# Kernel optimization log

Measured on AMD Instinct MI355X. Metric: run time of the kernel, lower is better.

## Reference

```python
import jax, jax.numpy as jnp
import numpy as np

N, H, L, S, E, D = 2, 8, 2048, 2048, 64, 64
C, K, BITS, ITERS = 128, 32, 32, 10
TEMP = 1.0 / np.sqrt(E)  # softmax_temp default 1/sqrt(E)


def setup_inputs() -> dict:
    key = jax.random.key(0)
    k1, k2, k3, k4 = jax.random.split(key, 4)
    return {
        "queries": jax.random.normal(k1, (N, L, H, E), jnp.float32),
        "keys": jax.random.normal(k2, (N, S, H, E), jnp.float32),
        "values": jax.random.normal(k3, (N, S, H, D), jnp.float32),
        "planes": jax.random.normal(k4, (BITS, E + 1), jnp.float32),
    }


def _cluster(bits):
    """K-means (Lloyd) on hamming distance over hash bits. bits: [N,H,L,B] in {0,1}."""
    qsum = bits.sum(-1)  # [N,H,L]
    idx0 = jnp.linspace(0, L - 1, C).astype(jnp.int32)  # deterministic centroid init
    cbits0 = bits[:, :, idx0, :]  # [N,H,C,B]

    def assign(cbits):
        # hamming(x,c) = sum(x) + sum(c) - 2*x.c  for 0/1 bits
        d = qsum[..., None] + cbits.sum(-1)[:, :, None, :] \
            - 2.0 * jnp.einsum('nhlb,nhcb->nhlc', bits, cbits)
        return jnp.argmin(d, -1)  # [N,H,L]

    def body(cbits, _):
        cl = assign(cbits)
        oh = jax.nn.one_hot(cl, C, dtype=bits.dtype)       # [N,H,L,C]
        counts = oh.sum(2)                                  # [N,H,C]
        bs = jnp.einsum('nhlc,nhlb->nhcb', oh, bits)        # per-cluster bit sums
        newc = (2.0 * bs > counts[..., None]).astype(bits.dtype)  # majority vote
        newc = jnp.where(counts[..., None] > 0, newc, cbits)      # keep empty clusters
        return newc, None

    cbits, _ = jax.lax.scan(body, cbits0, None, length=ITERS)
    cl = assign(cbits)
    counts = jax.nn.one_hot(cl, C, dtype=jnp.float32).sum(2)
    return cl, counts


def reference(queries, keys, values, planes):
    q = queries.transpose(0, 2, 1, 3)  # [N,H,L,E]
    k = keys.transpose(0, 2, 1, 3)     # [N,H,S,E]
    v = values.transpose(0, 2, 1, 3)   # [N,H,S,D]

    # LSH hashing of queries
    proj = jnp.einsum('nhle,be->nhlb', q, planes[:, :E]) + planes[:, E]
    bits = (proj > 0).astype(jnp.float32)
    cl, counts = _cluster(bits)  # [N,H,L], [N,H,C]

    sorted_indx = jnp.argsort(cl, axis=-1)
    sorted_cl = jnp.take_along_axis(cl, sorted_indx, -1)
    sq = jnp.take_along_axis(q, sorted_indx[..., None], 2)  # queries sorted by cluster

    # grouped queries = per-cluster mean
    counts_safe = jnp.maximum(counts, 1.0)
    oh = jax.nn.one_hot(cl, C, dtype=q.dtype)
    Qg = jnp.einsum('nhlc,nhle->nhce', oh, q) / counts_safe[..., None]

    # centroid-key dot products and top-k key selection per cluster
    QK = jnp.einsum('nhce,nhse->nhcs', Qg, k)  # [N,H,C,S]
    topk_values, topk = jax.lax.top_k(QK, K)   # [N,H,C,K]

    # bottom-k attention (dense per-cluster, top-k positions zeroed)
    A_full = jax.nn.softmax(TEMP * QK, -1)
    iN = jnp.arange(N)[:, None, None, None]
    iH = jnp.arange(H)[None, :, None, None]
    iC = jnp.arange(C)[None, None, :, None]
    mask = jnp.zeros_like(QK).at[iN, iH, iC, topk].set(1.0)
    A_b = A_full * (1.0 - mask)
    A_bottomk = A_b.sum(-1)                              # [N,H,C]
    Vb_g = jnp.einsum('nhcs,nhsd->nhcd', A_b, v)         # [N,H,C,D]
    Vb = jnp.take_along_axis(Vb_g, sorted_cl[..., None], 2)   # broadcast to queries
    A_bk_q = jnp.take_along_axis(A_bottomk, sorted_cl, 2)     # [N,H,L]

    # exact top-k attention per query
    topk_q = jnp.take_along_axis(topk, sorted_cl[..., None], 2)  # [N,H,L,K]
    gather = jax.vmap(jax.vmap(lambda t, i: t[i]))  # over N,H
    K_sel = gather(k, topk_q)  # [N,H,L,K,E]
    V_sel = gather(v, topk_q)  # [N,H,L,K,D]
    QKs = jnp.einsum('nhle,nhlke->nhlk', sq, K_sel)
    inf_mask = jnp.isinf(topk_values[:, 0, 0, :])  # [N,K] (padding sentinel; all False here)
    QKs = jnp.where(inf_mask[:, None, None, :], -jnp.inf, QKs)
    A_s = jax.nn.softmax(TEMP * QKs, -1) * (1.0 - A_bk_q[..., None])
    Vt = jnp.einsum('nhlk,nhlkd->nhld', A_s, V_sel)

    # combine and undo the cluster sort
    Vs = Vt + Vb
    rev = jnp.argsort(sorted_indx, -1)
    V_new = jnp.take_along_axis(Vs, rev[..., None], 2)
    sparse_index = jnp.take_along_axis(topk_q, rev[..., None], 2)
    A_topk = jnp.take_along_axis(A_s, rev[..., None], 2)
    return V_new.transpose(0, 2, 1, 3), sparse_index, A_topk
```

## Files before the change

### kernel.cpp

```cpp
#include <hip/hip_runtime.h>
#include <math.h>

constexpr int cN = 2, cH = 8, cL = 2048, cS = 2048, cE = 64, cD = 64;
constexpr int cC = 128, cK = 32, cB = 32, cIT = 10;
constexpr int cNH = cN * cH;
constexpr int SK = 8;
constexpr int CHUNK = cS / SK;
constexpr int NT = 16;
constexpr int HW = cC * 33;
constexpr int PARTSZ = 16;
constexpr int SLOTS = 256;
constexpr int NBUF = cIT + 1;

__global__ __launch_bounds__(256)
void k_bits(const float* __restrict__ q, const float* __restrict__ planes,
            unsigned int* __restrict__ bits, int* __restrict__ ghist)
{
    __shared__ float pl[cB * 68];
    int tid = threadIdx.x;
    for (int i = tid; i < cB * (cE + 1); i += 256) {
        int b = i / 65, e = i % 65;
        pl[b * 68 + e] = planes[i];
    }
    {
        const int ZS = NBUF * cNH * HW / 128;
        for (int i = tid; i < ZS; i += 256) ghist[(size_t)blockIdx.x * ZS + i] = 0;
    }
    __syncthreads();
    int idx = blockIdx.x * 256 + tid;
    int l = idx % cL, h = (idx / cL) % cH, n = idx / (cL * cH);
    const float* qr = q + (((size_t)n * cL + l) * cH + h) * cE;
    float qv[cE];
#pragma unroll
    for (int e4 = 0; e4 < cE / 4; ++e4) {
        float4 f = ((const float4*)qr)[e4];
        qv[4*e4+0] = f.x; qv[4*e4+1] = f.y; qv[4*e4+2] = f.z; qv[4*e4+3] = f.w;
    }
    unsigned int w = 0;
    for (int b = 0; b < cB; ++b) {
        const float4* pr = (const float4*)(pl + b * 68);
        float acc = 0.f;
#pragma unroll
        for (int e4 = 0; e4 < cE / 4; ++e4) {
            float4 f = pr[e4];
            acc = fmaf(qv[4*e4+0], f.x, acc);
            acc = fmaf(qv[4*e4+1], f.y, acc);
            acc = fmaf(qv[4*e4+2], f.z, acc);
            acc = fmaf(qv[4*e4+3], f.w, acc);
        }
        acc += pl[b * 68 + 64];
        if (acc > 0.f) w |= (1u << b);
    }
    bits[idx] = w;
}

__global__ __launch_bounds__(128)
void k_lloyd(const unsigned int* __restrict__ bits, int* __restrict__ ghist,
             unsigned int* __restrict__ cents, int* __restrict__ cl,
             int* __restrict__ pcounts, int it)
{
    __shared__ unsigned int scb[cC] __attribute__((aligned(16)));
    __shared__ int hist[HW];
    int tid = threadIdx.x, lane = tid & 63;
    int tile = blockIdx.x & (NT - 1), nh = blockIdx.x / NT;
    if (it == 0) {
        if (tid < cC) {
            int i0 = (int)(((double)tid * 2047.0) / 127.0);
            scb[tid] = bits[(size_t)nh * cL + i0];
        }
    } else {
        const unsigned int* cp = cents + (size_t)(it - 1) * cNH * cC + nh * cC;
        const int* gb = ghist + (size_t)((it - 1) * cNH + nh) * HW;
        if (tid < cC) {
            unsigned int oldc = cp[tid];
            int cnt = gb[4096 + tid];
            if (cnt > 0) {
                unsigned int nw = 0;
#pragma unroll
                for (int b = 0; b < cB; ++b)
                    if (2 * gb[tid * 32 + b] > cnt) nw |= (1u << b);
                oldc = nw;
            }
            scb[tid] = oldc;
        }
    }
    if (it < cIT) {
        for (int i = tid; i < HW; i += 128) hist[i] = 0;
    } else {
        hist[4096 + tid] = 0;
    }
    int l = tile * 128 + tid;
    unsigned int w = bits[(size_t)nh * cL + l];
    unsigned long long mymb = 0ull;
    if (it < cIT) {
#pragma unroll
        for (int b = 0; b < cB; ++b) {
            unsigned long long m = __ballot((w >> b) & 1u);
            if ((lane & 31) == b) mymb = m;
        }
    }
    __syncthreads();
    if (tile == 0 && it < cIT && tid < cC)
        cents[(size_t)it * cNH * cC + nh * cC + tid] = scb[tid];
    const uint4* scb4 = (const uint4*)scb;
    int b0 = 0x7fffffff, b1 = 0x7fffffff, b2 = 0x7fffffff, b3 = 0x7fffffff;
    for (int c4 = 0; c4 < cC / 4; ++c4) {
        uint4 cb = scb4[c4];
        int c = c4 * 4;
        b0 = min(b0, (__popc(w ^ cb.x) << 8) | c);
        b1 = min(b1, (__popc(w ^ cb.y) << 8) | (c + 1));
        b2 = min(b2, (__popc(w ^ cb.z) << 8) | (c + 2));
        b3 = min(b3, (__popc(w ^ cb.w) << 8) | (c + 3));
    }
    int best = min(min(b0, b1), min(b2, b3));
    int bc = best & 255;
    if (it == cIT) cl[(size_t)nh * cL + l] = bc;
    if (it < cIT) {
        unsigned long long rem = ~0ull;
        while (rem) {
            int src = __ffsll((long long)rem) - 1;
            int c = __shfl(bc, src);
            unsigned long long m = __ballot(bc == c);
            if (lane < cB) {
                int contrib = __popcll(m & mymb);
                if (contrib) atomicAdd(&hist[c * 32 + lane], contrib);
            }
            if (lane == 63) atomicAdd(&hist[4096 + c], __popcll(m));
            rem &= ~m;
        }
        __syncthreads();
        int* gb = ghist + (size_t)(it * cNH + nh) * HW;
        for (int i = tid; i < HW; i += 128) {
            int v = hist[i];
            if (v) atomicAdd(&gb[i], v);
        }
    } else {
        unsigned long long rem = ~0ull;
        while (rem) {
            int src = __ffsll((long long)rem) - 1;
            int c = __shfl(bc, src);
            unsigned long long m = __ballot(bc == c);
            if (lane == 63) atomicAdd(&hist[4096 + c], __popcll(m));
            rem &= ~m;
        }
        __syncthreads();
        pcounts[(nh * NT + tile) * cC + tid] = hist[4096 + tid];
    }
}

__global__ __launch_bounds__(128)
void k_rank(const int* __restrict__ cl, const int* __restrict__ pcounts,
            int* __restrict__ counts, int* __restrict__ moff,
            int* __restrict__ sched, int* __restrict__ mlist)
{
    __shared__ int pre[cC];
    __shared__ int scn[cC];
    __shared__ int sbefore[cC];
    __shared__ int wcnt0[cC];
    int tid = threadIdx.x, lane = tid & 63, wid = tid >> 6;
    int tile = blockIdx.x & (NT - 1), nh = blockIdx.x / NT;
    if (tid < cC) {
        int tot = 0, bef = 0;
        for (int t = 0; t < NT; ++t) {
            int v = pcounts[(nh * NT + t) * cC + tid];
            if (t < tile) bef += v;
            tot += v;
        }
        scn[tid] = tot;
        sbefore[tid] = bef;
    }
    __syncthreads();
    if (tid == 0) {
        int run = 0;
        for (int i = 0; i < cC; ++i) { pre[i] = run; run += scn[i]; }
    }
    __syncthreads();
    if (tile == 0) {
        if (tid < cC) {
            counts[nh * cC + tid] = scn[tid];
            moff[nh * cC + tid] = pre[tid];
        }
        sched[nh * SLOTS + tid] = -1;
        sched[nh * SLOTS + 128 + tid] = -1;
        __syncthreads();
        if (tid == 0) {
            int slot = 0;
            for (int i = 0; i < cC; ++i) {
                int np = (scn[i] + PARTSZ - 1) / PARTSZ;
                for (int p = 0; p < np; ++p)
                    sched[nh * SLOTS + slot++] = i | (p << 8);
            }
        }
    }
    int l = tile * 128 + tid;
    int bc = cl[(size_t)nh * cL + l];
    unsigned long long ltmask = (1ull << lane) - 1ull;
    int myrank = 0;
    for (int c = 0; c < cC; ++c) {
        unsigned long long m = __ballot(bc == c);
        if (wid == 0 && lane == 0) wcnt0[c] = __popcll(m);
        if (bc == c) myrank = __popcll(m & ltmask);
    }
    __syncthreads();
    int off = pre[bc] + sbefore[bc] + myrank + (wid == 1 ? wcnt0[bc] : 0);
    mlist[(size_t)nh * cL + off] = l;
}

__global__ __launch_bounds__(64)
void k_qg(const float* __restrict__ q, const int* __restrict__ mlist,
          const int* __restrict__ moff, const int* __restrict__ counts,
          float* __restrict__ Qg)
{
    int b = blockIdx.x;
    int nh = b >> 7;
    int h = nh % cH, n = nh / cH;
    int lane = threadIdx.x;
    int off = moff[b];
    int cnt = counts[b];
    const int* ml = mlist + (size_t)nh * cL + off;
    const float* qb = q + ((size_t)n * cL * cH + h) * cE + lane;
    float acc = 0.f;
    int j = 0;
    for (; j + 4 <= cnt; j += 4) {
        int i0 = ml[j], i1 = ml[j + 1], i2 = ml[j + 2], i3 = ml[j + 3];
        float v0 = qb[(size_t)i0 * cH * cE];
        float v1 = qb[(size_t)i1 * cH * cE];
        float v2 = qb[(size_t)i2 * cH * cE];
        float v3 = qb[(size_t)i3 * cH * cE];
        acc += v0; acc += v1; acc += v2; acc += v3;
    }
    for (; j < cnt; ++j) acc += qb[(size_t)ml[j] * cH * cE];
    float cs = (float)(cnt > 0 ? cnt : 1);
    Qg[(size_t)b * cE + lane] = acc / cs;
}

__global__ __launch_bounds__(256)
void k_qk_gemm(const float* __restrict__ key, const float* __restrict__ Qg,
               float* __restrict__ QK)
{
    __shared__ float qgT[cE][cC + 2];
    __shared__ float kT[cE][128 + 2];
    int tid = threadIdx.x;
    int bs = blockIdx.x & 15;
    int nh = blockIdx.x >> 4;
    int h = nh % cH, n = nh / cH;
    const float4* qsrc = (const float4*)(Qg + (size_t)nh * cC * cE);
#pragma unroll
    for (int i = 0; i < 8; ++i) {
        int f = tid + 256 * i;
        int c = f >> 4, e4 = (f & 15) << 2;
        float4 v = qsrc[f];
        qgT[e4+0][c] = v.x; qgT[e4+1][c] = v.y; qgT[e4+2][c] = v.z; qgT[e4+3][c] = v.w;
    }
    const float* kb = key + (size_t)n * cS * cH * cE + (size_t)h * cE;
    int s0 = bs * 128;
#pragma unroll
    for (int i = 0; i < 8; ++i) {
        int f = tid + 256 * i;
        int s = f >> 4, e4 = (f & 15) << 2;
        float4 v = *(const float4*)(kb + (size_t)(s0 + s) * (cH * cE) + e4);
        kT[e4+0][s] = v.x; kT[e4+1][s] = v.y; kT[e4+2][s] = v.z; kT[e4+3][s] = v.w;
    }
    __syncthreads();
    int tx = tid & 15, ty = tid >> 4;
    float acc[8][8];
#pragma unroll
    for (int i = 0; i < 8; ++i)
#pragma unroll
        for (int j = 0; j < 8; ++j) acc[i][j] = 0.f;
    for (int e = 0; e < cE; ++e) {
        float qv[8], kv[8];
#pragma unroll
        for (int i = 0; i < 8; ++i) qv[i] = qgT[e][ty + 16 * i];
#pragma unroll
        for (int j = 0; j < 8; ++j) kv[j] = kT[e][tx + 16 * j];
#pragma unroll
        for (int i = 0; i < 8; ++i)
#pragma unroll
            for (int j = 0; j < 8; ++j)
                acc[i][j] = fmaf(qv[i], kv[j], acc[i][j]);
    }
    float* dst = QK + (size_t)nh * cC * cS + s0;
#pragma unroll
    for (int i = 0; i < 8; ++i)
#pragma unroll
        for (int j = 0; j < 8; ++j)
            dst[(size_t)(ty + 16 * i) * cS + tx + 16 * j] = acc[i][j];
}

__global__ __launch_bounds__(256)
void k_sel(float* __restrict__ QK, int* __restrict__ topk,
           float* __restrict__ abk)
{
    __shared__ int sbins[4 * 257];
    __shared__ int ired[4];
    __shared__ float fred[4];
    __shared__ unsigned skey[cK];
    __shared__ float sval[cK];
    __shared__ int sidx[cK];
    __shared__ int stopk[cK];
    __shared__ int sDig, sRem, scnt;
    __shared__ float sM;
    int tid = threadIdx.x, lane = tid & 63, wid = tid >> 6;
    int b = blockIdx.x;
    float* qrow = QK + (size_t)b * cS;
    float v[8]; unsigned key[8];
#pragma unroll
    for (int j = 0; j < 8; ++j) {
        float f = qrow[tid + j * 256];
        v[j] = f;
        unsigned u = __float_as_uint(f);
        key[j] = (u & 0x80000000u) ? ~u : (u | 0x80000000u);
    }
    if (tid == 0) { sRem = cK; scnt = 0; }
    unsigned pfx = 0;
    for (int pass = 0; pass < 4; ++pass) {
        int sh = 24 - 8 * pass;
        for (int i = tid; i < 4 * 257; i += 256) sbins[i] = 0;
        __syncthreads();
        int rem = sRem;
#pragma unroll
        for (int j = 0; j < 8; ++j) {
            bool cand = (pass == 0) || ((key[j] >> (sh + 8)) == pfx);
            if (cand) atomicAdd(&sbins[wid * 257 + ((key[j] >> sh) & 255)], 1);
        }
        __syncthreads();
        if (wid == 0) {
            int d0 = lane * 4;
            int c0 = sbins[d0] + sbins[257 + d0] + sbins[514 + d0] + sbins[771 + d0];
            int c1 = sbins[d0+1] + sbins[257+d0+1] + sbins[514+d0+1] + sbins[771+d0+1];
            int c2 = sbins[d0+2] + sbins[257+d0+2] + sbins[514+d0+2] + sbins[771+d0+2];
            int c3 = sbins[d0+3] + sbins[257+d0+3] + sbins[514+d0+3] + sbins[771+d0+3];
            int tot = c0 + c1 + c2 + c3;
            int incl = tot;
#pragma unroll
            for (int off = 1; off < 64; off <<= 1) {
                int o = __shfl_down(incl, off);
                if (lane + off < 64) incl += o;
            }
            int sufHi = incl - tot;
            int G3 = sufHi, G2 = sufHi + c3, G1 = G2 + c2, G0 = G1 + c1;
            int hit = -1, hG = 0;
            if (G0 < rem && rem <= G0 + c0) { hit = d0 + 0; hG = G0; }
            if (G1 < rem && rem <= G1 + c1) { hit = d0 + 1; hG = G1; }
            if (G2 < rem && rem <= G2 + c2) { hit = d0 + 2; hG = G2; }
            if (G3 < rem && rem <= G3 + c3) { hit = d0 + 3; hG = G3; }
            unsigned long long m = __ballot(hit >= 0);
            int src = __ffsll((long long)m) - 1;
            int dsel = __shfl(hit, src);
            int Gsel = __shfl(hG, src);
            if (lane == 0) { sDig = dsel; sRem = rem - Gsel; }
        }
        __syncthreads();
        pfx = (pfx << 8) | (unsigned)sDig;
    }
    unsigned T = pfx;
    int need = sRem;
    int myT = 0;
#pragma unroll
    for (int j = 0; j < 8; ++j) myT += (key[j] == T);
#pragma unroll
    for (int off = 1; off < 64; off <<= 1) myT += __shfl_xor(myT, off);
    if (lane == 0) ired[wid] = myT;
    __syncthreads();
    int tieTot = ((ired[0] + ired[1]) + ired[2]) + ired[3];
    int tieCut = 0x7fffffff;
    if (tieTot != need) {
        int last = -1;
        for (int t = 0; t < need; ++t) {
            int mymin = 0x7fffffff;
#pragma unroll
            for (int j = 0; j < 8; ++j) {
                int idx = tid + j * 256;
                if (key[j] == T && idx > last) mymin = min(mymin, idx);
            }
#pragma unroll
            for (int off = 1; off < 64; off <<= 1)
                mymin = min(mymin, __shfl_xor(mymin, off));
            __syncthreads();
            if (lane == 0) ired[wid] = mymin;
            __syncthreads();
            last = min(min(ired[0], ired[1]), min(ired[2], ired[3]));
        }
        tieCut = last;
    }
    __syncthreads();
    int selm = 0;
#pragma unroll
    for (int j = 0; j < 8; ++j) {
        int idx = tid + j * 256;
        bool s_ = (key[j] > T) || (key[j] == T && idx <= tieCut);
        if (s_) {
            int slot = atomicAdd(&scnt, 1);
            skey[slot] = key[j]; sidx[slot] = idx; sval[slot] = v[j];
            selm |= (1 << j);
        }
    }
    __syncthreads();
    if (tid < cK) {
        unsigned kt = skey[tid]; int it = sidx[tid];
        int rank = 0;
#pragma unroll
        for (int j = 0; j < cK; ++j)
            rank += (skey[j] > kt) || (skey[j] == kt && sidx[j] < it);
        stopk[rank] = it;
        if (rank == 0) sM = sval[tid];
    }
    __syncthreads();
    if (tid < cK) topk[(size_t)b * cK + tid] = stopk[tid];
    float M = sM;
    float e8[8]; float ps = 0.f;
#pragma unroll
    for (int j = 0; j < 8; ++j) { e8[j] = expf(0.125f * (v[j] - M)); ps += e8[j]; }
#pragma unroll
    for (int off = 1; off < 64; off <<= 1) ps += __shfl_xor(ps, off);
    if (lane == 0) fred[wid] = ps;
    __syncthreads();
    float den = ((fred[0] + fred[1]) + fred[2]) + fred[3];
    float ab = 0.f;
#pragma unroll
    for (int j = 0; j < 8; ++j) {
        float P = (selm & (1 << j)) ? 0.f : e8[j] / den;
        ab += P;
        qrow[tid + j * 256] = P;
    }
#pragma unroll
    for (int off = 1; off < 64; off <<= 1) ab += __shfl_xor(ab, off);
    __syncthreads();
    if (lane == 0) fred[wid] = ab;
    __syncthreads();
    if (tid == 0) abk[b] = ((fred[0] + fred[1]) + fred[2]) + fred[3];
}

__global__ __launch_bounds__(256)
void k_pv(const float* __restrict__ P, const float* __restrict__ val,
          float* __restrict__ part)
{
    __shared__ float pT[64][64 + 2];
    __shared__ float vT[64][cD + 4];
    int tid = threadIdx.x;
    int ch = blockIdx.x & 1;
    int sk = (blockIdx.x >> 1) & 7;
    int nh = blockIdx.x >> 4;
    int h = nh % cH, n = nh / cH;
    int tx = tid & 15, ty = tid >> 4;
    float acc[4][4];
#pragma unroll
    for (int i = 0; i < 4; ++i)
#pragma unroll
        for (int j = 0; j < 4; ++j) acc[i][j] = 0.f;
    const float* pb = P + ((size_t)nh * cC + ch * 64) * cS;
    const float* vb = val + (size_t)n * cS * cH * cD + (size_t)h * cD;
    for (int sub = 0; sub < CHUNK / 64; ++sub) {
        int s0 = sk * CHUNK + sub * 64;
#pragma unroll
        for (int i = 0; i < 4; ++i) {
            int f = tid + 256 * i;
            int c = f >> 4, s4 = (f & 15) << 2;
            float4 v = *(const float4*)(pb + (size_t)c * cS + s0 + s4);
            pT[c][s4+0] = v.x; pT[c][s4+1] = v.y; pT[c][s4+2] = v.z; pT[c][s4+3] = v.w;
        }
#pragma unroll
        for (int i = 0; i < 4; ++i) {
            int f = tid + 256 * i;
            int ss = f >> 4, d4 = (f & 15) << 2;
            float4 v = *(const float4*)(vb + (size_t)(s0 + ss) * (cH * cD) + d4);
            vT[ss][d4+0] = v.x; vT[ss][d4+1] = v.y; vT[ss][d4+2] = v.z; vT[ss][d4+3] = v.w;
        }
        __syncthreads();
        for (int ss = 0; ss < 64; ++ss) {
            float pv[4];
#pragma unroll
            for (int i = 0; i < 4; ++i) pv[i] = pT[ty + 16 * i][ss];
            float4 vv = *(const float4*)&vT[ss][tx * 4];
#pragma unroll
            for (int i = 0; i < 4; ++i) {
                acc[i][0] = fmaf(pv[i], vv.x, acc[i][0]);
                acc[i][1] = fmaf(pv[i], vv.y, acc[i][1]);
                acc[i][2] = fmaf(pv[i], vv.z, acc[i][2]);
                acc[i][3] = fmaf(pv[i], vv.w, acc[i][3]);
            }
        }
        __syncthreads();
    }
    float* dst = part + (((size_t)sk * cNH + nh) * cC + ch * 64) * cD;
#pragma unroll
    for (int i = 0; i < 4; ++i) {
        float4 o; o.x = acc[i][0]; o.y = acc[i][1]; o.z = acc[i][2]; o.w = acc[i][3];
        *(float4*)(dst + (size_t)(ty + 16 * i) * cD + tx * 4) = o;
    }
}

__global__ __launch_bounds__(256)
void k_out(const float* __restrict__ q, const float* __restrict__ key,
           const float* __restrict__ val, const int* __restrict__ mlist,
           const int* __restrict__ moff, const int* __restrict__ counts,
           const float* __restrict__ abk, const float* __restrict__ part,
           const int* __restrict__ topk, const int* __restrict__ sched,
           float* __restrict__ out)
{
    __shared__ float vlds[cK][cD + 1];
    __shared__ float aslds[4][cK];
    __shared__ int   st[cK];
    int tid = threadIdx.x, lane = tid & 63, wid = tid >> 6;
    int nh = blockIdx.x >> 8;
    int slot = blockIdx.x & 255;
    int item = sched[nh * SLOTS + slot];
    if (item < 0) return;
    int c = item & 255, part_i = item >> 8;
    int b = nh * cC + c;
    int h = nh % cH, n = nh / cH;
    if (tid < cK) st[tid] = topk[(size_t)b * cK + tid];
    __syncthreads();
    const float* kb = key + ((size_t)n * cS * cH + h) * cE;
    const float* vb = val + ((size_t)n * cS * cH + h) * cD;
    for (int r = wid; r < cK; r += 4)
        vlds[r][lane] = vb[(size_t)st[r] * cH * cD + lane];
    int k = lane >> 1, hh = lane & 1;
    float4 kreg[8];
    {
        const float* kr = kb + (size_t)st[k] * cH * cE + hh * 32;
#pragma unroll
        for (int j = 0; j < 8; ++j) kreg[j] = ((const float4*)kr)[j];
    }
    float vbgd = 0.f;
    {
        const float* pp = part + (size_t)b * cD + lane;
#pragma unroll
        for (int sk = 0; sk < SK; ++sk)
            vbgd += pp[(size_t)sk * (cNH * cC * cD)];
    }
    __syncthreads();
    int cnt = counts[b];
    int off = moff[b];
    float scale = 1.0f - abk[b];
    float stf = (lane < cK) ? (float)st[lane] : 0.f;
    const int* ml = mlist + (size_t)nh * cL + off;
    const size_t off1 = (size_t)cN * cL * cH * cD;
    const size_t off2 = off1 + (size_t)cN * cH * cL * cK;
    int mstart = part_i * PARTSZ;
    int mend = min(mstart + PARTSZ, cnt);
    for (int m = mstart + wid; m < mend; m += 4) {
        int l = ml[m];
        const float* qrow = q + (((size_t)n * cL + l) * cH + h) * cE + hh * 32;
        float4 qf[8];
#pragma unroll
        for (int j = 0; j < 8; ++j) qf[j] = ((const float4*)qrow)[j];
        float partial = 0.f;
#pragma unroll
        for (int j = 0; j < 8; ++j) {
            partial = fmaf(qf[j].x, kreg[j].x, partial);
            partial = fmaf(qf[j].y, kreg[j].y, partial);
            partial = fmaf(qf[j].z, kreg[j].z, partial);
            partial = fmaf(qf[j].w, kreg[j].w, partial);
        }
        float qk = partial + __shfl_xor(partial, 1);
        float M = qk;
#pragma unroll
        for (int o = 2; o < 64; o <<= 1) M = fmaxf(M, __shfl_xor(M, o));
        float ev = expf(0.125f * (qk - M));
        float den = ev;
#pragma unroll
        for (int o = 2; o < 64; o <<= 1) den += __shfl_xor(den, o);
        float as_ = (ev / den) * scale;
        if (!hh) aslds[wid][k] = as_;
        float acc = 0.f;
#pragma unroll
        for (int j = 0; j < cK; ++j)
            acc = fmaf(aslds[wid][j], vlds[j][lane], acc);
        acc += vbgd;
        int qidx = nh * cL + l;
        out[(((size_t)n * cL + l) * cH + h) * cD + lane] = acc;
        if (lane < cK) {
            out[off1 + (size_t)qidx * cK + lane] = stf;
            out[off2 + (size_t)qidx * cK + lane] = aslds[wid][lane];
        }
    }
}

extern "C" void kernel_launch(void* const* d_in, const int* in_sizes, int n_in,
                              void* d_out, int out_size, void* d_ws, size_t ws_size,
                              hipStream_t stream)
{
    (void)in_sizes; (void)n_in; (void)out_size; (void)ws_size;
    const float* q      = (const float*)d_in[0];
    const float* key    = (const float*)d_in[1];
    const float* val    = (const float*)d_in[2];
    const float* planes = (const float*)d_in[3];
    char* w = (char*)d_ws;
    unsigned int* bits = (unsigned int*)w;  w += (size_t)cN * cH * cL * 4;
    int*   cl     = (int*)w;                w += (size_t)cN * cH * cL * 4;
    int*   counts = (int*)w;                w += (size_t)cN * cH * cC * 4;
    float* abk    = (float*)w;              w += (size_t)cN * cH * cC * 4;
    float* Qg     = (float*)w;              w += (size_t)cN * cH * cC * cE * 4;
    int*   topkp  = (int*)w;                w += (size_t)cN * cH * cC * cK * 4;
    float* QK     = (float*)w;              w += (size_t)cNH * cC * cS * 4;
    float* part   = (float*)w;              w += (size_t)SK * cNH * cC * cD * 4;
    int*   ghist  = (int*)w;                w += (size_t)NBUF * cNH * HW * 4;
    unsigned int* cents = (unsigned int*)w; w += (size_t)NBUF * cNH * cC * 4;
    int*   pcounts= (int*)w;                w += (size_t)cNH * NT * cC * 4;
    int*   mlist  = (int*)w;                w += (size_t)cNH * cL * 4;
    int*   moff   = (int*)w;                w += (size_t)cNH * cC * 4;
    int*   sched  = (int*)w;                w += (size_t)cNH * SLOTS * 4;
    float* out = (float*)d_out;

    k_bits <<<(cN * cH * cL) / 256, 256, 0, stream>>>(q, planes, bits, ghist);
    for (int it = 0; it <= cIT; ++it)
        k_lloyd <<<cNH * NT, 128, 0, stream>>>(bits, ghist, cents, cl, pcounts, it);
    k_rank <<<cNH * NT, 128, 0, stream>>>(cl, pcounts, counts, moff, sched, mlist);
    k_qg     <<<cNH * cC, 64, 0, stream>>>(q, mlist, moff, counts, Qg);
    k_qk_gemm<<<cNH * 16, 256, 0, stream>>>(key, Qg, QK);
    k_sel    <<<cNH * cC, 256, 0, stream>>>(QK, topkp, abk);
    k_pv     <<<cNH * SK * 2, 256, 0, stream>>>(QK, val, part);
    k_out    <<<cNH * SLOTS, 256, 0, stream>>>(q, key, val, mlist, moff, counts,
                                               abk, part, topkp, sched, out);
}
```

Measured before the change: 309.7 us.

## Widen clustering blocks, use ballot-loop ranking, drop split-cluster output schedule

The Lloyd and rank kernels now run 256 threads per block over 8 tiles instead of 128 threads over 16 tiles. The rank kernel replaces its loop over all 128 clusters with a loop over only the distinct cluster ids found in each wave, keeping per-wave counts for the prefix offsets. The serial single-thread schedule build is removed, and the output kernel now launches one block per cluster that walks every member, instead of splitting large clusters into 16-query parts. This cuts launch and serial scheduling overhead, but it risks load imbalance in the output kernel when clusters are large.

Measured after the change: 274.5 us, median of 2. -11.3%, faster.

```diff
diff --git a/kernel.cpp b/kernel.cpp
--- a/kernel.cpp
+++ b/kernel.cpp
@@ -6,10 +6,8 @@
 constexpr int cNH = cN * cH;
 constexpr int SK = 8;
 constexpr int CHUNK = cS / SK;
-constexpr int NT = 16;
+constexpr int NT = 8;
 constexpr int HW = cC * 33;
-constexpr int PARTSZ = 16;
-constexpr int SLOTS = 256;
 constexpr int NBUF = cIT + 1;
 
 __global__ __launch_bounds__(256)
@@ -54,7 +52,7 @@
     bits[idx] = w;
 }
 
-__global__ __launch_bounds__(128)
+__global__ __launch_bounds__(256)
 void k_lloyd(const unsigned int* __restrict__ bits, int* __restrict__ ghist,
              unsigned int* __restrict__ cents, int* __restrict__ cl,
              int* __restrict__ pcounts, int it)
@@ -85,11 +83,11 @@
         }
     }
     if (it < cIT) {
-        for (int i = tid; i < HW; i += 128) hist[i] = 0;
+        for (int i = tid; i < HW; i += 256) hist[i] = 0;
     } else {
-        hist[4096 + tid] = 0;
-    }
-    int l = tile * 128 + tid;
+        if (tid < cC) hist[4096 + tid] = 0;
+    }
+    int l = tile * 256 + tid;
     unsigned int w = bits[(size_t)nh * cL + l];
     unsigned long long mymb = 0ull;
     if (it < cIT) {
@@ -130,7 +128,7 @@
         }
         __syncthreads();
         int* gb = ghist + (size_t)(it * cNH + nh) * HW;
-        for (int i = tid; i < HW; i += 128) {
+        for (int i = tid; i < HW; i += 256) {
             int v = hist[i];
             if (v) atomicAdd(&gb[i], v);
         }
@@ -144,19 +142,19 @@
             rem &= ~m;
         }
         __syncthreads();
-        pcounts[(nh * NT + tile) * cC + tid] = hist[4096 + tid];
-    }
-}
-
-__global__ __launch_bounds__(128)
+        if (tid < cC) pcounts[(nh * NT + tile) * cC + tid] = hist[4096 + tid];
+    }
+}
+
+__global__ __launch_bounds__(256)
 void k_rank(const int* __restrict__ cl, const int* __restrict__ pcounts,
             int* __restrict__ counts, int* __restrict__ moff,
-            int* __restrict__ sched, int* __restrict__ mlist)
+            int* __restrict__ mlist)
 {
     __shared__ int pre[cC];
     __shared__ int scn[cC];
     __shared__ int sbefore[cC];
-    __shared__ int wcnt0[cC];
+    __shared__ int wcnt[4][cC];
     int tid = threadIdx.x, lane = tid & 63, wid = tid >> 6;
     int tile = blockIdx.x & (NT - 1), nh = blockIdx.x / NT;
     if (tid < cC) {
@@ -169,6 +167,10 @@
         scn[tid] = tot;
         sbefore[tid] = bef;
     }
+    {
+        int* wf = &wcnt[0][0];
+        for (int i = tid; i < 4 * cC; i += 256) wf[i] = 0;
+    }
     __syncthreads();
     if (tid == 0) {
         int run = 0;
@@ -180,29 +182,26 @@
             counts[nh * cC + tid] = scn[tid];
             moff[nh * cC + tid] = pre[tid];
         }
-        sched[nh * SLOTS + tid] = -1;
-        sched[nh * SLOTS + 128 + tid] = -1;
-        __syncthreads();
-        if (tid == 0) {
-            int slot = 0;
-            for (int i = 0; i < cC; ++i) {
-                int np = (scn[i] + PARTSZ - 1) / PARTSZ;
-                for (int p = 0; p < np; ++p)
-                    sched[nh * SLOTS + slot++] = i | (p << 8);
-            }
-        }
-    }
-    int l = tile * 128 + tid;
+    }
+    int l = tile * 256 + tid;
     int bc = cl[(size_t)nh * cL + l];
     unsigned long long ltmask = (1ull << lane) - 1ull;
     int myrank = 0;
-    for (int c = 0; c < cC; ++c) {
-        unsigned long long m = __ballot(bc == c);
-        if (wid == 0 && lane == 0) wcnt0[c] = __popcll(m);
-        if (bc == c) myrank = __popcll(m & ltmask);
-    }
-    __syncthreads();
-    int off = pre[bc] + sbefore[bc] + myrank + (wid == 1 ? wcnt0[bc] : 0);
+    {
+        unsigned long long rem = ~0ull;
+        while (rem) {
+            int src = __ffsll((long long)rem) - 1;
+            int c = __shfl(bc, src);
+            unsigned long long m = __ballot(bc == c);
+            if (lane == 0) wcnt[wid][c] = __popcll(m);
+            if (bc == c) myrank = __popcll(m & ltmask);
+            rem &= ~m;
+        }
+    }
+    __syncthreads();
+    int off = pre[bc] + sbefore[bc] + myrank;
+    for (int w2 = 0; w2 < 4; ++w2)
+        if (w2 < wid) off += wcnt[w2][bc];
     mlist[(size_t)nh * cL + off] = l;
 }
 
@@ -496,19 +495,14 @@
            const float* __restrict__ val, const int* __restrict__ mlist,
            const int* __restrict__ moff, const int* __restrict__ counts,
            const float* __restrict__ abk, const float* __restrict__ part,
-           const int* __restrict__ topk, const int* __restrict__ sched,
-           float* __restrict__ out)
+           const int* __restrict__ topk, float* __restrict__ out)
 {
     __shared__ float vlds[cK][cD + 1];
     __shared__ float aslds[4][cK];
     __shared__ int   st[cK];
     int tid = threadIdx.x, lane = tid & 63, wid = tid >> 6;
-    int nh = blockIdx.x >> 8;
-    int slot = blockIdx.x & 255;
-    int item = sched[nh * SLOTS + slot];
-    if (item < 0) return;
-    int c = item & 255, part_i = item >> 8;
-    int b = nh * cC + c;
+    int b = blockIdx.x;
+    int nh = b >> 7;
     int h = nh % cH, n = nh / cH;
     if (tid < cK) st[tid] = topk[(size_t)b * cK + tid];
     __syncthreads();
@@ -538,9 +532,7 @@
     const int* ml = mlist + (size_t)nh * cL + off;
     const size_t off1 = (size_t)cN * cL * cH * cD;
     const size_t off2 = off1 + (size_t)cN * cH * cL * cK;
-    int mstart = part_i * PARTSZ;
-    int mend = min(mstart + PARTSZ, cnt);
-    for (int m = mstart + wid; m < mend; m += 4) {
+    for (int m = wid; m < cnt; m += 4) {
         int l = ml[m];
         const float* qrow = q + (((size_t)n * cL + l) * cH + h) * cE + hh * 32;
         float4 qf[8];
@@ -601,17 +593,16 @@
     int*   pcounts= (int*)w;                w += (size_t)cNH * NT * cC * 4;
     int*   mlist  = (int*)w;                w += (size_t)cNH * cL * 4;
     int*   moff   = (int*)w;                w += (size_t)cNH * cC * 4;
-    int*   sched  = (int*)w;                w += (size_t)cNH * SLOTS * 4;
     float* out = (float*)d_out;
 
     k_bits <<<(cN * cH * cL) / 256, 256, 0, stream>>>(q, planes, bits, ghist);
     for (int it = 0; it <= cIT; ++it)
-        k_lloyd <<<cNH * NT, 128, 0, stream>>>(bits, ghist, cents, cl, pcounts, it);
-    k_rank <<<cNH * NT, 128, 0, stream>>>(cl, pcounts, counts, moff, sched, mlist);
+        k_lloyd <<<cNH * NT, 256, 0, stream>>>(bits, ghist, cents, cl, pcounts, it);
+    k_rank <<<cNH * NT, 256, 0, stream>>>(cl, pcounts, counts, moff, mlist);
     k_qg     <<<cNH * cC, 64, 0, stream>>>(q, mlist, moff, counts, Qg);
     k_qk_gemm<<<cNH * 16, 256, 0, stream>>>(key, Qg, QK);
     k_sel    <<<cNH * cC, 256, 0, stream>>>(QK, topkp, abk);
     k_pv     <<<cNH * SK * 2, 256, 0, stream>>>(QK, val, part);
-    k_out    <<<cNH * SLOTS, 256, 0, stream>>>(q, key, val, mlist, moff, counts,
-                                               abk, part, topkp, sched, out);
-}
+    k_out    <<<cNH * cC, 256, 0, stream>>>(q, key, val, mlist, moff, counts,
+                                            abk, part, topkp, out);
+}
```
